# Performance work log

Hardware: AMD Instinct MI355X
Metric: run time of the kernel (lower is better)

## Reference

```python
import jax, jax.numpy as jnp
import numpy as np

B, N, S, D, K = 8, 8192, 2048, 256, 3
MLP = [256, 128]
EPS = 1e-5


def setup_inputs() -> dict:
    key = jax.random.key(0)
    ks = jax.random.split(key, 12)
    inp = {
        "xyz1": jax.random.normal(ks[0], (B, N, 3), dtype=jnp.float32),
        "xyz2": jax.random.normal(ks[1], (B, S, 3), dtype=jnp.float32),
        "points1": jax.random.normal(ks[2], (B, N, D), dtype=jnp.float32),
        "points2": jax.random.normal(ks[3], (B, S, D), dtype=jnp.float32),
        # relation conv: Conv2d(4 -> 1, kernel 1x1) == linear over last dim
        "rel_w": jax.random.normal(ks[4], (4,), dtype=jnp.float32) * 0.5,
        "rel_b": jnp.zeros((), dtype=jnp.float32),
        # mlp layer 0: Conv1d(2D -> 256, k=1) + BN
        "W0": jax.random.normal(ks[5], (MLP[0], 2 * D), dtype=jnp.float32) * (1.0 / np.sqrt(2 * D)),
        "b0": jnp.zeros((MLP[0],), dtype=jnp.float32),
        "g0": jnp.ones((MLP[0],), dtype=jnp.float32),
        "be0": jnp.zeros((MLP[0],), dtype=jnp.float32),
        # mlp layer 1: Conv1d(256 -> 128, k=1) + BN
        "W1": jax.random.normal(ks[6], (MLP[1], MLP[0]), dtype=jnp.float32) * (1.0 / np.sqrt(MLP[0])),
        "b1": jnp.zeros((MLP[1],), dtype=jnp.float32),
        "g1": jnp.ones((MLP[1],), dtype=jnp.float32),
        "be1": jnp.zeros((MLP[1],), dtype=jnp.float32),
    }
    return inp


def _gather(points, idx):
    # points: [B,S,C], idx: [B,N,K] -> [B,N,K,C]
    return jax.vmap(lambda p, i: p[i])(points, idx)


def _bn_relu(x, gamma, beta):
    # training-mode BatchNorm1d over [B,N,C]: stats over (B,N), biased var
    mean = jnp.mean(x, axis=(0, 1))
    var = jnp.var(x, axis=(0, 1))
    xn = (x - mean) * jax.lax.rsqrt(var + EPS)
    return jax.nn.relu(xn * gamma + beta)


def reference(xyz1, xyz2, points1, points2, rel_w, rel_b,
              W0, b0, g0, be0, W1, b1, g1, be1):
    # pairwise squared distances [B,N,S]
    d = (jnp.sum(xyz1 ** 2, -1)[:, :, None]
         + jnp.sum(xyz2 ** 2, -1)[:, None, :]
         - 2.0 * jnp.einsum('bnc,bmc->bnm', xyz1, xyz2))
    neg_d, idx = jax.lax.top_k(-d, K)          # K smallest distances
    dists = -neg_d                              # [B,N,K]

    offset = xyz1[:, :, None, :] - _gather(xyz2, idx)        # [B,N,K,3]
    rel = jnp.concatenate([dists[..., None], offset], -1)    # [B,N,K,4]
    weight = jax.nn.sigmoid(rel @ rel_w + rel_b)              # [B,N,K]

    interp = jnp.mean(_gather(points2, idx) * weight[..., None], axis=2)  # [B,N,D]
    h = jnp.concatenate([points1, interp], axis=-1)           # [B,N,2D]

    h = _bn_relu(jnp.einsum('bnc,oc->bno', h, W0) + b0, g0, be0)
    h = _bn_relu(jnp.einsum('bnc,oc->bno', h, W1) + b1, g1, be1)
    return h  # [B,N,128]
```

## Files before the change

kernel.cpp:

```cpp
#include <hip/hip_runtime.h>
#include <stdint.h>
#include <stddef.h>

#define B_   8
#define N_   8192
#define S_   2048
#define D_   256
#define M_   (B_*N_)
#define C0_  256
#define C1_  128
#define K2D_ 512
#define TS_  4
#define SEG_ (S_/TS_)

typedef __attribute__((ext_vector_type(8))) short short8;
typedef __attribute__((ext_vector_type(4))) short short4v;
typedef __attribute__((ext_vector_type(4))) float f32x4;
typedef __attribute__((ext_vector_type(2))) float f32x2;

__device__ __forceinline__ short f2bf(float f) {
  unsigned u = __float_as_uint(f);
  u += 0x7fffu + ((u >> 16) & 1u);
  return (short)(u >> 16);
}
__device__ __forceinline__ float bf2f(short s) {
  return __uint_as_float(((unsigned)(unsigned short)s) << 16);
}

__device__ __forceinline__ void cp16(const void* g, void* l) {
  __builtin_amdgcn_global_load_lds(
      (__attribute__((address_space(1))) void*)(g),
      (__attribute__((address_space(3))) void*)(l), 16, 0, 0);
}

__global__ void convw_kernel(const float* __restrict__ W0,
                             const float* __restrict__ W1,
                             const float* __restrict__ xyz2,
                             short* __restrict__ W0b, short* __restrict__ W1b,
                             float* __restrict__ xyz2p, float* __restrict__ stats) {
  int i = blockIdx.x * 256 + threadIdx.x;
  if (blockIdx.x == 0) {
    stats[threadIdx.x] = 0.f;
    stats[256 + threadIdx.x] = 0.f;
    stats[512 + threadIdx.x] = 0.f;
  }
  if (i < C0_ * K2D_) W0b[i] = f2bf(W0[i]);
  if (i < C1_ * C0_)  W1b[i] = f2bf(W1[i]);
  if (i < B_ * S_) {
    const int b = i >> 11, s = i & (S_ - 1);
    float x = xyz2[(size_t)i * 3 + 0];
    float y = xyz2[(size_t)i * 3 + 1];
    float z = xyz2[(size_t)i * 3 + 2];
    float ss = __fadd_rn(__fadd_rn(__fmul_rn(x, x), __fmul_rn(y, y)), __fmul_rn(z, z));
    float* xw = xyz2p + (size_t)b * 4 * S_;
    xw[s] = x; xw[S_ + s] = y; xw[2 * S_ + s] = z; xw[3 * S_ + s] = ss;
  }
}

__global__ __launch_bounds__(256, 1)
void topk_kernel(const float* __restrict__ xyz1, const float* __restrict__ xyz2p,
                 const float* __restrict__ relw, const float* __restrict__ relb,
                 int* __restrict__ idx_out, float* __restrict__ w_out) {
  __shared__ float cd[TS_][64][3];
  __shared__ int   ci[TS_][64][3];
  const int tid  = threadIdx.x;
  const int lane = tid & 63;
  const int seg  = __builtin_amdgcn_readfirstlane(tid >> 6);
  const int b    = blockIdx.x >> 7;
  const int n    = (blockIdx.x & 127) * 64 + lane;

  const float* p = xyz1 + ((size_t)b * N_ + n) * 3;
  const float ax = p[0], ay = p[1], az = p[2];
  const float s1 = __fadd_rn(__fadd_rn(__fmul_rn(ax, ax), __fmul_rn(ay, ay)), __fmul_rn(az, az));

  const float* xw = xyz2p + (size_t)b * 4 * S_;
  const f32x2* XP = (const f32x2*)(xw)           + seg * (SEG_ / 2);
  const f32x2* YP = (const f32x2*)(xw + S_)      + seg * (SEG_ / 2);
  const f32x2* ZP = (const f32x2*)(xw + 2 * S_)  + seg * (SEG_ / 2);
  const f32x2* WP = (const f32x2*)(xw + 3 * S_)  + seg * (SEG_ / 2);

  float d0 = 3.4e38f, d1 = 3.4e38f, d2 = 3.4e38f;
  int   i0 = 0, i1 = 0, i2 = 0;
  const int sbeg = seg * SEG_;
  {
    #pragma clang fp contract(off)
    #pragma unroll 4
    for (int pr = 0; pr < SEG_ / 2; pr++) {
      f32x2 X = XP[pr], Y = YP[pr], Z = ZP[pr], W = WP[pr];
      f32x2 t1 = ax * X;
      f32x2 t2 = ay * Y;
      f32x2 t3 = az * Z;
      f32x2 dt = (t1 + t2) + t3;
      f32x2 e  = s1 + W;
      f32x2 m  = 2.0f * dt;
      f32x2 d  = e - m;
      const float dlo = d.x, dhi = d.y;
      if (fminf(dlo, dhi) < d2) {
        const int s = sbeg + 2 * pr;
        if (dlo < d2) {
          if (dlo < d1) {
            d2 = d1; i2 = i1;
            if (dlo < d0) { d1 = d0; i1 = i0; d0 = dlo; i0 = s; }
            else          { d1 = dlo; i1 = s; }
          } else { d2 = dlo; i2 = s; }
        }
        if (dhi < d2) {
          if (dhi < d1) {
            d2 = d1; i2 = i1;
            if (dhi < d0) { d1 = d0; i1 = i0; d0 = dhi; i0 = s + 1; }
            else          { d1 = dhi; i1 = s + 1; }
          } else { d2 = dhi; i2 = s + 1; }
        }
      }
    }
  }
  cd[seg][lane][0] = d0; cd[seg][lane][1] = d1; cd[seg][lane][2] = d2;
  ci[seg][lane][0] = i0; ci[seg][lane][1] = i1; ci[seg][lane][2] = i2;
  __syncthreads();

  if (tid < 64) {
    float m0 = 3.4e38f, m1 = 3.4e38f, m2 = 3.4e38f;
    int   j0 = 0, j1 = 0, j2 = 0;
    #pragma unroll
    for (int sg = 0; sg < TS_; sg++) {
      #pragma unroll
      for (int k = 0; k < 3; k++) {
        float d = cd[sg][tid][k];
        int   ix = ci[sg][tid][k];
        if (d < m2) {
          if (d < m1) {
            m2 = m1; j2 = j1;
            if (d < m0) { m1 = m0; j1 = j0; m0 = d; j0 = ix; }
            else        { m1 = d;  j1 = ix; }
          } else { m2 = d; j2 = ix; }
        }
      }
    }
    const float w0r = relw[0], w1r = relw[1], w2r = relw[2], w3r = relw[3], br = relb[0];
    const size_t base = ((size_t)b * N_ + n) * 3;
    float dd[3] = {m0, m1, m2};
    int   ii[3] = {j0, j1, j2};
    #pragma unroll
    for (int k = 0; k < 3; k++) {
      const int s = ii[k];
      float ox = ax - xw[s], oy = ay - xw[S_ + s], oz = az - xw[2 * S_ + s];
      float t = dd[k] * w0r + ox * w1r + oy * w2r + oz * w3r + br;
      float w = 1.0f / (1.0f + expf(-t));
      idx_out[base + k] = s;
      w_out[base + k] = w * (1.0f / 3.0f);
    }
  }
}

__global__ __launch_bounds__(256, 1)
void build_h_kernel(const float* __restrict__ p1, const float* __restrict__ p2,
                    const int* __restrict__ idx, const float* __restrict__ wts,
                    short* __restrict__ h) {
  const int tid = threadIdx.x;
  const int row = blockIdx.x * 4 + (tid >> 6);
  const int cl = (tid & 63) * 4;
  const int b = row >> 13;
  const int i0 = idx[row * 3 + 0], i1 = idx[row * 3 + 1], i2 = idx[row * 3 + 2];
  const float w0 = wts[row * 3 + 0], w1 = wts[row * 3 + 1], w2 = wts[row * 3 + 2];
  const float* pb = p2 + (size_t)b * S_ * D_;
  float4 a  = *(const float4*)(p1 + (size_t)row * D_ + cl);
  float4 v0 = *(const float4*)(pb + (size_t)i0 * D_ + cl);
  float4 v1 = *(const float4*)(pb + (size_t)i1 * D_ + cl);
  float4 v2 = *(const float4*)(pb + (size_t)i2 * D_ + cl);
  short4v o1 = { f2bf(a.x), f2bf(a.y), f2bf(a.z), f2bf(a.w) };
  short4v o2 = { f2bf(w0 * v0.x + w1 * v1.x + w2 * v2.x),
                 f2bf(w0 * v0.y + w1 * v1.y + w2 * v2.y),
                 f2bf(w0 * v0.z + w1 * v1.z + w2 * v2.z),
                 f2bf(w0 * v0.w + w1 * v1.w + w2 * v2.w) };
  *(short4v*)(h + (size_t)row * K2D_ + cl)       = o1;
  *(short4v*)(h + (size_t)row * K2D_ + D_ + cl)  = o2;
}

template <int KTOT>
__global__ __launch_bounds__(256, 1)
void gemm_bt_kernel(const short* __restrict__ A, const short* __restrict__ Bw,
                    const float* __restrict__ bias, short* __restrict__ Cb,
                    float* __restrict__ stats, const int Nout) {
  __shared__ __align__(16) short sA[128 * 32];
  __shared__ __align__(16) short sB[128 * 32];
  const int tid = threadIdx.x;
  const int lane = tid & 63;
  const int wave = tid >> 6;
  const int wm = wave & 1;
  const int wn = wave >> 1;
  const size_t mbase = (size_t)blockIdx.x * 128;
  const int nbase = blockIdx.y * 128;

  const int lrow = lane >> 2;
  const int lcol = (lane & 3) * 8;

  f32x4 acc[4][4] = {};

  for (int k0 = 0; k0 < KTOT; k0 += 32) {
    #pragma unroll
    for (int t = 0; t < 2; t++) {
      const int r = wave * 32 + t * 16;
      cp16(A  + (mbase + r + lrow) * KTOT + k0 + lcol, &sA[r * 32]);
      cp16(Bw + (size_t)(nbase + r + lrow) * KTOT + k0 + lcol, &sB[r * 32]);
    }
    __syncthreads();

    const int mr = lane & 15;
    const int ks = (lane >> 4) * 8;
    short8 af[4], bfr[4];
    #pragma unroll
    for (int i = 0; i < 4; i++) af[i]  = *(const short8*)&sA[(wm * 64 + i * 16 + mr) * 32 + ks];
    #pragma unroll
    for (int j = 0; j < 4; j++) bfr[j] = *(const short8*)&sB[(wn * 64 + j * 16 + mr) * 32 + ks];
    #pragma unroll
    for (int i = 0; i < 4; i++)
      #pragma unroll
      for (int j = 0; j < 4; j++)
        acc[i][j] = __builtin_amdgcn_mfma_f32_16x16x32_bf16(af[i], bfr[j], acc[i][j], 0, 0, 0);
    __syncthreads();
  }

  const int cr = (lane >> 4) * 4;
  const int cc = lane & 15;
  float ps[4], ps2[4];
  #pragma unroll
  for (int j = 0; j < 4; j++) {
    const int col = nbase + wn * 64 + j * 16 + cc;
    const float bv = bias[col];
    float s = 0.f, s2 = 0.f;
    #pragma unroll
    for (int i = 0; i < 4; i++) {
      #pragma unroll
      for (int r = 0; r < 4; r++) {
        const float v = acc[i][j][r];
        s += v; s2 += v * v;
        const size_t row = mbase + wm * 64 + i * 16 + cr + r;
        Cb[row * Nout + col] = f2bf(v + bv);
      }
    }
    ps[j] = s; ps2[j] = s2;
  }
  #pragma unroll
  for (int j = 0; j < 4; j++) {
    ps[j]  += __shfl_xor(ps[j], 16);  ps[j]  += __shfl_xor(ps[j], 32);
    ps2[j] += __shfl_xor(ps2[j], 16); ps2[j] += __shfl_xor(ps2[j], 32);
  }
  float* sred = (float*)sA;
  if (wm == 1 && lane < 16) {
    #pragma unroll
    for (int j = 0; j < 4; j++) {
      const int c = wn * 64 + j * 16 + lane;
      sred[2 * c] = ps[j]; sred[2 * c + 1] = ps2[j];
    }
  }
  __syncthreads();
  if (wm == 0 && lane < 16) {
    #pragma unroll
    for (int j = 0; j < 4; j++) {
      const int c = wn * 64 + j * 16 + lane;
      atomicAdd(&stats[nbase + c],        ps[j]  + sred[2 * c]);
      atomicAdd(&stats[Nout + nbase + c], ps2[j] + sred[2 * c + 1]);
    }
  }
}

__global__ void stats_final_kernel(const float* __restrict__ stats, const int C,
                                   const float* __restrict__ bias,
                                   const float* __restrict__ g, const float* __restrict__ be,
                                   float* __restrict__ ss) {
  const int c = threadIdx.x;
  if (c >= C) return;
  const float inv = 1.0f / (float)M_;
  float m0 = stats[c] * inv;
  float var = stats[C + c] * inv - m0 * m0;
  float mean = m0 + bias[c];
  float sc = g[c] * rsqrtf(var + 1e-5f);
  ss[c] = sc;
  ss[C + c] = be[c] - mean * sc;
}

__global__ __launch_bounds__(256, 1)
void norm1_kernel(const short* __restrict__ a1, const float* __restrict__ ss,
                  short* __restrict__ h1) {
  const size_t t = (size_t)blockIdx.x * 256 + threadIdx.x;
  const size_t base = t * 8;
  const int c = (int)(base & (C0_ - 1));
  short8 v8 = *(const short8*)(a1 + base);
  short8 o;
  #pragma unroll
  for (int k = 0; k < 8; k++) {
    float v = bf2f(v8[k]) * ss[c + k] + ss[C0_ + c + k];
    o[k] = f2bf(v > 0.f ? v : 0.f);
  }
  *(short8*)(h1 + base) = o;
}

__global__ __launch_bounds__(256, 1)
void norm2_kernel(const short* __restrict__ a2, const float* __restrict__ ss,
                  float* __restrict__ out) {
  const size_t t = (size_t)blockIdx.x * 256 + threadIdx.x;
  const size_t base = t * 8;
  const int c = (int)(base & (C1_ - 1));
  short8 v8 = *(const short8*)(a2 + base);
  float vv[8];
  #pragma unroll
  for (int k = 0; k < 8; k++) {
    float v = bf2f(v8[k]) * ss[c + k] + ss[C1_ + c + k];
    vv[k] = v > 0.f ? v : 0.f;
  }
  *(float4*)(out + base)     = make_float4(vv[0], vv[1], vv[2], vv[3]);
  *(float4*)(out + base + 4) = make_float4(vv[4], vv[5], vv[6], vv[7]);
}

extern "C" void kernel_launch(void* const* d_in, const int* in_sizes, int n_in,
                              void* d_out, int out_size, void* d_ws, size_t ws_size,
                              hipStream_t stream) {
  const float* xyz1 = (const float*)d_in[0];
  const float* xyz2 = (const float*)d_in[1];
  const float* pts1 = (const float*)d_in[2];
  const float* pts2 = (const float*)d_in[3];
  const float* relw = (const float*)d_in[4];
  const float* relb = (const float*)d_in[5];
  const float* W0   = (const float*)d_in[6];
  const float* b0   = (const float*)d_in[7];
  const float* g0   = (const float*)d_in[8];
  const float* be0  = (const float*)d_in[9];
  const float* W1   = (const float*)d_in[10];
  const float* b1   = (const float*)d_in[11];
  const float* g1   = (const float*)d_in[12];
  const float* be1  = (const float*)d_in[13];

  char* ws = (char*)d_ws;
  constexpr size_t IDX_OFF = 0;
  constexpr size_t WTS_OFF = IDX_OFF + (size_t)M_ * 3 * 4;
  constexpr size_t W0B_OFF = WTS_OFF + (size_t)M_ * 3 * 4;
  constexpr size_t W1B_OFF = W0B_OFF + (size_t)C0_ * K2D_ * 2;
  constexpr size_t XW_OFF  = W1B_OFF + (size_t)C1_ * C0_ * 2;
  constexpr size_t H_OFF   = XW_OFF + (size_t)B_ * 4 * S_ * 4;
  constexpr size_t A1_OFF  = H_OFF + (size_t)M_ * K2D_ * 2;
  constexpr size_t H1_OFF  = A1_OFF + (size_t)M_ * C0_ * 2;
  constexpr size_t A2_OFF  = H1_OFF + (size_t)M_ * C0_ * 2;
  constexpr size_t ST_OFF  = A2_OFF + (size_t)M_ * C1_ * 2;
  constexpr size_t SS1_OFF = ST_OFF + (size_t)768 * 4;
  constexpr size_t SS2_OFF = SS1_OFF + (size_t)2 * C0_ * 4;

  int*   idx   = (int*)(ws + IDX_OFF);
  float* wts   = (float*)(ws + WTS_OFF);
  short* W0b   = (short*)(ws + W0B_OFF);
  short* W1b   = (short*)(ws + W1B_OFF);
  float* xyz2p = (float*)(ws + XW_OFF);
  short* h     = (short*)(ws + H_OFF);
  short* a1    = (short*)(ws + A1_OFF);
  short* h1    = (short*)(ws + H1_OFF);
  short* a2    = (short*)(ws + A2_OFF);
  float* st    = (float*)(ws + ST_OFF);
  float* ss1   = (float*)(ws + SS1_OFF);
  float* ss2   = (float*)(ws + SS2_OFF);
  float* outp  = (float*)d_out;

  convw_kernel<<<512, 256, 0, stream>>>(W0, W1, xyz2, W0b, W1b, xyz2p, st);
  topk_kernel<<<B_ * (N_ / 64), 256, 0, stream>>>(xyz1, xyz2p, relw, relb, idx, wts);
  build_h_kernel<<<M_ / 4, 256, 0, stream>>>(pts1, pts2, idx, wts, h);

  gemm_bt_kernel<K2D_><<<dim3(M_ / 128, C0_ / 128), 256, 0, stream>>>(h, W0b, b0, a1, st, C0_);
  stats_final_kernel<<<1, 256, 0, stream>>>(st, C0_, b0, g0, be0, ss1);
  norm1_kernel<<<(size_t)M_ * C0_ / 8 / 256, 256, 0, stream>>>(a1, ss1, h1);

  gemm_bt_kernel<C0_><<<dim3(M_ / 128, C1_ / 128), 256, 0, stream>>>(h1, W1b, b1, a2, st + 512, C1_);
  stats_final_kernel<<<1, 128, 0, stream>>>(st + 512, C1_, b1, g1, be1, ss2);
  norm2_kernel<<<(size_t)M_ * C1_ / 8 / 256, 256, 0, stream>>>(a2, ss2, outp);
}
```

Baseline: 320.9 us.

## Fuse gather-interpolation into GEMM1 and BN1 normalize into GEMM2, widen top-k

The separate build_h and norm1 kernels are removed. GEMM1 now builds its A tile directly from points1 and the weighted three-neighbor gather of points2, converting to bf16 in registers. GEMM2 applies the layer-0 BN scale/shift and ReLU while loading its A tile. Together these avoid writing and re-reading the h and h1 intermediates. The top-k kernel is also split into 8 segments with 512 threads per block and a higher occupancy hint. In exchange, the fused A loads go through registers instead of async LDS copies, and GEMM1 re-gathers the points2 rows once per output column block (twice in total).

```diff
diff --git a/kernel.cpp b/kernel.cpp
--- a/kernel.cpp
+++ b/kernel.cpp
@@ -10,8 +10,8 @@
 #define C0_  256
 #define C1_  128
 #define K2D_ 512
-#define TS_  4
-#define SEG_ (S_/TS_)
+#define TS8_ 8
+#define SEG8_ (S_/TS8_)
 
 typedef __attribute__((ext_vector_type(8))) short short8;
 typedef __attribute__((ext_vector_type(4))) short short4v;
@@ -57,12 +57,12 @@
   }
 }
 
-__global__ __launch_bounds__(256, 1)
+__global__ __launch_bounds__(512, 8)
 void topk_kernel(const float* __restrict__ xyz1, const float* __restrict__ xyz2p,
                  const float* __restrict__ relw, const float* __restrict__ relb,
                  int* __restrict__ idx_out, float* __restrict__ w_out) {
-  __shared__ float cd[TS_][64][3];
-  __shared__ int   ci[TS_][64][3];
+  __shared__ float cd[TS8_][64][3];
+  __shared__ int   ci[TS8_][64][3];
   const int tid  = threadIdx.x;
   const int lane = tid & 63;
   const int seg  = __builtin_amdgcn_readfirstlane(tid >> 6);
@@ -74,18 +74,18 @@
   const float s1 = __fadd_rn(__fadd_rn(__fmul_rn(ax, ax), __fmul_rn(ay, ay)), __fmul_rn(az, az));
 
   const float* xw = xyz2p + (size_t)b * 4 * S_;
-  const f32x2* XP = (const f32x2*)(xw)           + seg * (SEG_ / 2);
-  const f32x2* YP = (const f32x2*)(xw + S_)      + seg * (SEG_ / 2);
-  const f32x2* ZP = (const f32x2*)(xw + 2 * S_)  + seg * (SEG_ / 2);
-  const f32x2* WP = (const f32x2*)(xw + 3 * S_)  + seg * (SEG_ / 2);
+  const f32x2* XP = (const f32x2*)(xw)           + seg * (SEG8_ / 2);
+  const f32x2* YP = (const f32x2*)(xw + S_)      + seg * (SEG8_ / 2);
+  const f32x2* ZP = (const f32x2*)(xw + 2 * S_)  + seg * (SEG8_ / 2);
+  const f32x2* WP = (const f32x2*)(xw + 3 * S_)  + seg * (SEG8_ / 2);
 
   float d0 = 3.4e38f, d1 = 3.4e38f, d2 = 3.4e38f;
   int   i0 = 0, i1 = 0, i2 = 0;
-  const int sbeg = seg * SEG_;
+  const int sbeg = seg * SEG8_;
   {
     #pragma clang fp contract(off)
     #pragma unroll 4
-    for (int pr = 0; pr < SEG_ / 2; pr++) {
+    for (int pr = 0; pr < SEG8_ / 2; pr++) {
       f32x2 X = XP[pr], Y = YP[pr], Z = ZP[pr], W = WP[pr];
       f32x2 t1 = ax * X;
       f32x2 t2 = ay * Y;
@@ -122,7 +122,7 @@
     float m0 = 3.4e38f, m1 = 3.4e38f, m2 = 3.4e38f;
     int   j0 = 0, j1 = 0, j2 = 0;
     #pragma unroll
-    for (int sg = 0; sg < TS_; sg++) {
+    for (int sg = 0; sg < TS8_; sg++) {
       #pragma unroll
       for (int k = 0; k < 3; k++) {
         float d = cd[sg][tid][k];
@@ -152,35 +152,11 @@
   }
 }
 
-__global__ __launch_bounds__(256, 1)
-void build_h_kernel(const float* __restrict__ p1, const float* __restrict__ p2,
-                    const int* __restrict__ idx, const float* __restrict__ wts,
-                    short* __restrict__ h) {
-  const int tid = threadIdx.x;
-  const int row = blockIdx.x * 4 + (tid >> 6);
-  const int cl = (tid & 63) * 4;
-  const int b = row >> 13;
-  const int i0 = idx[row * 3 + 0], i1 = idx[row * 3 + 1], i2 = idx[row * 3 + 2];
-  const float w0 = wts[row * 3 + 0], w1 = wts[row * 3 + 1], w2 = wts[row * 3 + 2];
-  const float* pb = p2 + (size_t)b * S_ * D_;
-  float4 a  = *(const float4*)(p1 + (size_t)row * D_ + cl);
-  float4 v0 = *(const float4*)(pb + (size_t)i0 * D_ + cl);
-  float4 v1 = *(const float4*)(pb + (size_t)i1 * D_ + cl);
-  float4 v2 = *(const float4*)(pb + (size_t)i2 * D_ + cl);
-  short4v o1 = { f2bf(a.x), f2bf(a.y), f2bf(a.z), f2bf(a.w) };
-  short4v o2 = { f2bf(w0 * v0.x + w1 * v1.x + w2 * v2.x),
-                 f2bf(w0 * v0.y + w1 * v1.y + w2 * v2.y),
-                 f2bf(w0 * v0.z + w1 * v1.z + w2 * v2.z),
-                 f2bf(w0 * v0.w + w1 * v1.w + w2 * v2.w) };
-  *(short4v*)(h + (size_t)row * K2D_ + cl)       = o1;
-  *(short4v*)(h + (size_t)row * K2D_ + D_ + cl)  = o2;
-}
-
-template <int KTOT>
-__global__ __launch_bounds__(256, 1)
-void gemm_bt_kernel(const short* __restrict__ A, const short* __restrict__ Bw,
-                    const float* __restrict__ bias, short* __restrict__ Cb,
-                    float* __restrict__ stats, const int Nout) {
+__global__ __launch_bounds__(256, 3)
+void gemm1_kernel(const float* __restrict__ p1, const float* __restrict__ p2,
+                  const int* __restrict__ idx, const float* __restrict__ wts,
+                  const short* __restrict__ Bw, const float* __restrict__ bias,
+                  short* __restrict__ Cb, float* __restrict__ stats) {
   __shared__ __align__(16) short sA[128 * 32];
   __shared__ __align__(16) short sB[128 * 32];
   const int tid = threadIdx.x;
@@ -190,18 +166,49 @@
   const int wn = wave >> 1;
   const size_t mbase = (size_t)blockIdx.x * 128;
   const int nbase = blockIdx.y * 128;
-
   const int lrow = lane >> 2;
   const int lcol = (lane & 3) * 8;
 
   f32x4 acc[4][4] = {};
 
-  for (int k0 = 0; k0 < KTOT; k0 += 32) {
+  for (int k0 = 0; k0 < K2D_; k0 += 32) {
     #pragma unroll
     for (int t = 0; t < 2; t++) {
       const int r = wave * 32 + t * 16;
-      cp16(A  + (mbase + r + lrow) * KTOT + k0 + lcol, &sA[r * 32]);
-      cp16(Bw + (size_t)(nbase + r + lrow) * KTOT + k0 + lcol, &sB[r * 32]);
+      const int row = (int)mbase + r + lrow;
+      cp16(Bw + (size_t)(nbase + r + lrow) * K2D_ + k0 + lcol, &sB[r * 32]);
+      float v[8];
+      if (k0 < D_) {
+        const float* src = p1 + (size_t)row * D_ + k0 + lcol;
+        float4 f0 = *(const float4*)src;
+        float4 f1 = *(const float4*)(src + 4);
+        v[0] = f0.x; v[1] = f0.y; v[2] = f0.z; v[3] = f0.w;
+        v[4] = f1.x; v[5] = f1.y; v[6] = f1.z; v[7] = f1.w;
+      } else {
+        const int c2 = k0 - D_ + lcol;
+        const int bb = row >> 13;
+        const float* pb = p2 + (size_t)bb * S_ * D_;
+        const int i0 = idx[row * 3 + 0], i1 = idx[row * 3 + 1], i2 = idx[row * 3 + 2];
+        const float w0 = wts[row * 3 + 0], w1 = wts[row * 3 + 1], w2 = wts[row * 3 + 2];
+        const float* q0 = pb + (size_t)i0 * D_ + c2;
+        const float* q1 = pb + (size_t)i1 * D_ + c2;
+        const float* q2 = pb + (size_t)i2 * D_ + c2;
+        float4 a0 = *(const float4*)q0, a1v = *(const float4*)(q0 + 4);
+        float4 b0 = *(const float4*)q1, b1v = *(const float4*)(q1 + 4);
+        float4 c0 = *(const float4*)q2, c1v = *(const float4*)(q2 + 4);
+        v[0] = w0 * a0.x + w1 * b0.x + w2 * c0.x;
+        v[1] = w0 * a0.y + w1 * b0.y + w2 * c0.y;
+        v[2] = w0 * a0.z + w1 * b0.z + w2 * c0.z;
+        v[3] = w0 * a0.w + w1 * b0.w + w2 * c0.w;
+        v[4] = w0 * a1v.x + w1 * b1v.x + w2 * c1v.x;
+        v[5] = w0 * a1v.y + w1 * b1v.y + w2 * c1v.y;
+        v[6] = w0 * a1v.z + w1 * b1v.z + w2 * c1v.z;
+        v[7] = w0 * a1v.w + w1 * b1v.w + w2 * c1v.w;
+      }
+      short8 o;
+      #pragma unroll
+      for (int e = 0; e < 8; e++) o[e] = f2bf(v[e]);
+      *(short8*)&sA[(r + lrow) * 32 + lcol] = o;
     }
     __syncthreads();
 
@@ -235,7 +242,7 @@
         const float v = acc[i][j][r];
         s += v; s2 += v * v;
         const size_t row = mbase + wm * 64 + i * 16 + cr + r;
-        Cb[row * Nout + col] = f2bf(v + bv);
+        Cb[row * C0_ + col] = f2bf(v + bv);
       }
     }
     ps[j] = s; ps2[j] = s2;
@@ -258,8 +265,107 @@
     #pragma unroll
     for (int j = 0; j < 4; j++) {
       const int c = wn * 64 + j * 16 + lane;
-      atomicAdd(&stats[nbase + c],        ps[j]  + sred[2 * c]);
-      atomicAdd(&stats[Nout + nbase + c], ps2[j] + sred[2 * c + 1]);
+      atomicAdd(&stats[nbase + c],       ps[j]  + sred[2 * c]);
+      atomicAdd(&stats[C0_ + nbase + c], ps2[j] + sred[2 * c + 1]);
+    }
+  }
+}
+
+__global__ __launch_bounds__(256, 2)
+void gemm2_kernel(const short* __restrict__ A, const short* __restrict__ Bw,
+                  const float* __restrict__ ssn, const float* __restrict__ bias,
+                  short* __restrict__ Cb, float* __restrict__ stats) {
+  __shared__ __align__(16) short sA[128 * 32];
+  __shared__ __align__(16) short sB[128 * 32];
+  const int tid = threadIdx.x;
+  const int lane = tid & 63;
+  const int wave = tid >> 6;
+  const int wm = wave & 1;
+  const int wn = wave >> 1;
+  const size_t mbase = (size_t)blockIdx.x * 128;
+  const int lrow = lane >> 2;
+  const int lcol = (lane & 3) * 8;
+
+  f32x4 acc[4][4] = {};
+
+  for (int k0 = 0; k0 < C0_; k0 += 32) {
+    float4 sca = *(const float4*)(ssn + k0 + lcol);
+    float4 scb = *(const float4*)(ssn + k0 + lcol + 4);
+    float4 sha = *(const float4*)(ssn + C0_ + k0 + lcol);
+    float4 shb = *(const float4*)(ssn + C0_ + k0 + lcol + 4);
+    #pragma unroll
+    for (int t = 0; t < 2; t++) {
+      const int r = wave * 32 + t * 16;
+      const int row = (int)mbase + r + lrow;
+      cp16(Bw + (size_t)(r + lrow) * C0_ + k0 + lcol, &sB[r * 32]);
+      short8 av = *(const short8*)(A + (size_t)row * C0_ + k0 + lcol);
+      float sc[8] = {sca.x, sca.y, sca.z, sca.w, scb.x, scb.y, scb.z, scb.w};
+      float sh[8] = {sha.x, sha.y, sha.z, sha.w, shb.x, shb.y, shb.z, shb.w};
+      short8 o;
+      #pragma unroll
+      for (int e = 0; e < 8; e++) {
+        float v = bf2f(av[e]) * sc[e] + sh[e];
+        o[e] = f2bf(v > 0.f ? v : 0.f);
+      }
+      *(short8*)&sA[(r + lrow) * 32 + lcol] = o;
+    }
+    __syncthreads();
+
+    const int mr = lane & 15;
+    const int ks = (lane >> 4) * 8;
+    short8 af[4], bfr[4];
+    #pragma unroll
+    for (int i = 0; i < 4; i++) af[i]  = *(const short8*)&sA[(wm * 64 + i * 16 + mr) * 32 + ks];
+    #pragma unroll
+    for (int j = 0; j < 4; j++) bfr[j] = *(const short8*)&sB[(wn * 64 + j * 16 + mr) * 32 + ks];
+    #pragma unroll
+    for (int i = 0; i < 4; i++)
+      #pragma unroll
+      for (int j = 0; j < 4; j++)
+        acc[i][j] = __builtin_amdgcn_mfma_f32_16x16x32_bf16(af[i], bfr[j], acc[i][j], 0, 0, 0);
+    __syncthreads();
+  }
+
+  const int cr = (lane >> 4) * 4;
+  const int cc = lane & 15;
+  float ps[4], ps2[4];
+  #pragma unroll
+  for (int j = 0; j < 4; j++) {
+    const int col = wn * 64 + j * 16 + cc;
+    const float bv = bias[col];
+    float s = 0.f, s2 = 0.f;
+    #pragma unroll
+    for (int i = 0; i < 4; i++) {
+      #pragma unroll
+      for (int r = 0; r < 4; r++) {
+        const float v = acc[i][j][r];
+        s += v; s2 += v * v;
+        const size_t row = mbase + wm * 64 + i * 16 + cr + r;
+        Cb[row * C1_ + col] = f2bf(v + bv);
+      }
+    }
+    ps[j] = s; ps2[j] = s2;
+  }
+  #pragma unroll
+  for (int j = 0; j < 4; j++) {
+    ps[j]  += __shfl_xor(ps[j], 16);  ps[j]  += __shfl_xor(ps[j], 32);
+    ps2[j] += __shfl_xor(ps2[j], 16); ps2[j] += __shfl_xor(ps2[j], 32);
+  }
+  float* sred = (float*)sA;
+  if (wm == 1 && lane < 16) {
+    #pragma unroll
+    for (int j = 0; j < 4; j++) {
+      const int c = wn * 64 + j * 16 + lane;
+      sred[2 * c] = ps[j]; sred[2 * c + 1] = ps2[j];
+    }
+  }
+  __syncthreads();
+  if (wm == 0 && lane < 16) {
+    #pragma unroll
+    for (int j = 0; j < 4; j++) {
+      const int c = wn * 64 + j * 16 + lane;
+      atomicAdd(&stats[c],       ps[j]  + sred[2 * c]);
+      atomicAdd(&stats[C1_ + c], ps2[j] + sred[2 * c + 1]);
     }
   }
 }
@@ -277,22 +383,6 @@
   float sc = g[c] * rsqrtf(var + 1e-5f);
   ss[c] = sc;
   ss[C + c] = be[c] - mean * sc;
-}
-
-__global__ __launch_bounds__(256, 1)
-void norm1_kernel(const short* __restrict__ a1, const float* __restrict__ ss,
-                  short* __restrict__ h1) {
-  const size_t t = (size_t)blockIdx.x * 256 + threadIdx.x;
-  const size_t base = t * 8;
-  const int c = (int)(base & (C0_ - 1));
-  short8 v8 = *(const short8*)(a1 + base);
-  short8 o;
-  #pragma unroll
-  for (int k = 0; k < 8; k++) {
-    float v = bf2f(v8[k]) * ss[c + k] + ss[C0_ + c + k];
-    o[k] = f2bf(v > 0.f ? v : 0.f);
-  }
-  *(short8*)(h1 + base) = o;
 }
 
 __global__ __launch_bounds__(256, 1)
@@ -336,10 +426,8 @@
   constexpr size_t W0B_OFF = WTS_OFF + (size_t)M_ * 3 * 4;
   constexpr size_t W1B_OFF = W0B_OFF + (size_t)C0_ * K2D_ * 2;
   constexpr size_t XW_OFF  = W1B_OFF + (size_t)C1_ * C0_ * 2;
-  constexpr size_t H_OFF   = XW_OFF + (size_t)B_ * 4 * S_ * 4;
-  constexpr size_t A1_OFF  = H_OFF + (size_t)M_ * K2D_ * 2;
-  constexpr size_t H1_OFF  = A1_OFF + (size_t)M_ * C0_ * 2;
-  constexpr size_t A2_OFF  = H1_OFF + (size_t)M_ * C0_ * 2;
+  constexpr size_t A1_OFF  = XW_OFF + (size_t)B_ * 4 * S_ * 4;
+  constexpr size_t A2_OFF  = A1_OFF + (size_t)M_ * C0_ * 2;
   constexpr size_t ST_OFF  = A2_OFF + (size_t)M_ * C1_ * 2;
   constexpr size_t SS1_OFF = ST_OFF + (size_t)768 * 4;
   constexpr size_t SS2_OFF = SS1_OFF + (size_t)2 * C0_ * 4;
@@ -349,9 +437,7 @@
   short* W0b   = (short*)(ws + W0B_OFF);
   short* W1b   = (short*)(ws + W1B_OFF);
   float* xyz2p = (float*)(ws + XW_OFF);
-  short* h     = (short*)(ws + H_OFF);
   short* a1    = (short*)(ws + A1_OFF);
-  short* h1    = (short*)(ws + H1_OFF);
   short* a2    = (short*)(ws + A2_OFF);
   float* st    = (float*)(ws + ST_OFF);
   float* ss1   = (float*)(ws + SS1_OFF);
@@ -359,14 +445,13 @@
   float* outp  = (float*)d_out;
 
   convw_kernel<<<512, 256, 0, stream>>>(W0, W1, xyz2, W0b, W1b, xyz2p, st);
-  topk_kernel<<<B_ * (N_ / 64), 256, 0, stream>>>(xyz1, xyz2p, relw, relb, idx, wts);
-  build_h_kernel<<<M_ / 4, 256, 0, stream>>>(pts1, pts2, idx, wts, h);
-
-  gemm_bt_kernel<K2D_><<<dim3(M_ / 128, C0_ / 128), 256, 0, stream>>>(h, W0b, b0, a1, st, C0_);
+  topk_kernel<<<B_ * (N_ / 64), 512, 0, stream>>>(xyz1, xyz2p, relw, relb, idx, wts);
+
+  gemm1_kernel<<<dim3(M_ / 128, C0_ / 128), 256, 0, stream>>>(
+      pts1, pts2, idx, wts, W0b, b0, a1, st);
   stats_final_kernel<<<1, 256, 0, stream>>>(st, C0_, b0, g0, be0, ss1);
-  norm1_kernel<<<(size_t)M_ * C0_ / 8 / 256, 256, 0, stream>>>(a1, ss1, h1);
-
-  gemm_bt_kernel<C0_><<<dim3(M_ / 128, C1_ / 128), 256, 0, stream>>>(h1, W1b, b1, a2, st + 512, C1_);
+
+  gemm2_kernel<<<dim3(M_ / 128, 1), 256, 0, stream>>>(a1, W1b, ss1, b1, a2, st + 512);
   stats_final_kernel<<<1, 128, 0, stream>>>(st + 512, C1_, b1, g1, be1, ss2);
   norm2_kernel<<<(size_t)M_ * C1_ / 8 / 256, 256, 0, stream>>>(a2, ss2, outp);
 }
```

Measured after the change: 306.0 us. 1.05x faster.
